# Kernel optimization log

Hardware: AMD Instinct MI355X
Metric: run time of the kernel (lower is better)

## Reference

```python
import jax, jax.numpy as jnp
import numpy as np

T, B, D, H, L = 64, 512, 1536, 1024, 4
DISCOUNT = 0.997
LAM = 0.95


def setup_inputs() -> dict:
    key = jax.random.key(0)
    ks = jax.random.split(key, 3 + L + 1)
    inp = {
        'feat': jax.random.normal(ks[0], (T, B, D), dtype=jnp.float32),
        'reward': jax.random.normal(ks[1], (T - 1, B), dtype=jnp.float32),
        'cont': jnp.ones((T, B), dtype=jnp.float32),
    }
    scale = 0.02
    dims = [D] + [H] * L
    for i in range(L):
        inp[f'W{i}'] = jax.random.normal(ks[3 + i], (dims[i], dims[i + 1]), dtype=jnp.float32) * scale
        inp[f'b{i}'] = jnp.zeros((dims[i + 1],), dtype=jnp.float32)
    inp['Wo'] = jax.random.normal(ks[3 + L], (H,), dtype=jnp.float32) * scale
    inp['bo'] = jnp.zeros((), dtype=jnp.float32)
    return inp


def reference(feat, reward, cont, W0, b0, W1, b1, W2, b2, W3, b3, Wo, bo):
    # Value-net MLP (mean of critic dist): [T, B, D] -> [T, B]
    h = feat
    for W, b in ((W0, b0), (W1, b1), (W2, b2), (W3, b3)):
        h = jax.nn.silu(h @ W + b)
    value = h @ Wo + bo  # [T, B]

    disc = cont[1:] * DISCOUNT                      # [T-1, B]
    deltas = reward + disc * value[1:] - value[:-1]  # [T-1, B]

    # GAE: adv_t = delta_t + disc_t * lambda * adv_{t+1}, adv_T = 0
    def step(adv_next, xs):
        delta, dl = xs
        adv = delta + dl * adv_next
        return adv, adv

    _, advs = jax.lax.scan(step, jnp.zeros_like(value[0]),
                           (deltas, disc * LAM), reverse=True)
    ret = advs + value[:-1]   # lambda-return target, [T-1, B]
    baseline = value[:-1]
    return ret, baseline
```

## Files before the change

### kernel.cpp

```cpp
#include <hip/hip_runtime.h>
#include <hip/hip_bf16.h>

#define T_DIM 64
#define B_DIM 512
#define D_DIM 1536
#define H_DIM 1024
#define M_DIM (T_DIM * B_DIM)
#define DISCOUNT 0.997f
#define LAM 0.95f

#define BM 256
#define BN 256
#define BK 32
#define TILES_M (M_DIM / BM)
#define TILES_N (H_DIM / BN)
#define N_XCD 8

typedef __bf16 bf16x8 __attribute__((ext_vector_type(8)));
typedef float  f32x4  __attribute__((ext_vector_type(4)));

__device__ __forceinline__ void async_load16(const void* g, void* l) {
    __builtin_amdgcn_global_load_lds(
        (const __attribute__((address_space(1))) void*)g,
        (__attribute__((address_space(3))) void*)l,
        16, 0, 0);
}

__device__ __forceinline__ unsigned short f2bf_raw(float f) {
    __hip_bfloat16 h = __float2bfloat16(f);
    return *reinterpret_cast<unsigned short*>(&h);
}

__global__ __launch_bounds__(256) void cvt_bf16_kernel(
    const float* __restrict__ x, __hip_bfloat16* __restrict__ y, long n4) {
    long i = (long)blockIdx.x * blockDim.x + threadIdx.x;
    if (i >= n4) return;
    float4 v = reinterpret_cast<const float4*>(x)[i];
    ushort4 o;
    o.x = f2bf_raw(v.x);
    o.y = f2bf_raw(v.y);
    o.z = f2bf_raw(v.z);
    o.w = f2bf_raw(v.w);
    reinterpret_cast<ushort4*>(y)[i] = o;
}

__global__ __launch_bounds__(256) void transpose_cvt_all_kernel(
    const float* __restrict__ W0, const float* __restrict__ W1,
    const float* __restrict__ W2, const float* __restrict__ W3,
    __hip_bfloat16* __restrict__ T0, __hip_bfloat16* __restrict__ T1,
    __hip_bfloat16* __restrict__ T2, __hip_bfloat16* __restrict__ T3) {
    __shared__ float tile[32][33];
    int z = blockIdx.z;
    const float* W;
    __hip_bfloat16* Tt;
    int K;
    if (z == 0)      { W = W0; Tt = T0; K = D_DIM; }
    else if (z == 1) { W = W1; Tt = T1; K = H_DIM; }
    else if (z == 2) { W = W2; Tt = T2; K = H_DIM; }
    else             { W = W3; Tt = T3; K = H_DIM; }
    int k0 = blockIdx.x * 32, n0 = blockIdx.y * 32;
    if (k0 >= K) return;
    int tx = threadIdx.x, ty = threadIdx.y;
    #pragma unroll
    for (int r = ty; r < 32; r += 8)
        tile[r][tx] = W[(size_t)(k0 + r) * H_DIM + n0 + tx];
    __syncthreads();
    #pragma unroll
    for (int r = ty; r < 32; r += 8)
        Tt[(size_t)(n0 + r) * K + k0 + tx] = __float2bfloat16(tile[tx][r]);
}

__global__ __launch_bounds__(512, 2) void gemm_silu_kernel(
    const __hip_bfloat16* __restrict__ A,
    const __hip_bfloat16* __restrict__ Bt,
    const float* __restrict__ bias,
    __hip_bfloat16* __restrict__ C,
    int K) {

    __shared__ alignas(16) __hip_bfloat16 lds[65536];

    const int tid  = threadIdx.x;
    const int wave = tid >> 6;
    const int lane = tid & 63;
    const int quad = lane >> 4;
    const int r16  = lane & 15;
    const int wm   = wave & 1;
    const int wn   = wave >> 1;

    const int l     = blockIdx.x;
    const int xcd   = l & (N_XCD - 1);
    const int local = l >> 3;
    const int tn    = local & (TILES_N - 1);
    const int tm    = (xcd << 4) | (local >> 2);
    const int m0 = tm * BM;
    const int n0 = tn * BN;

    const int rsub = lane >> 2;
    const int cgrp = lane & 3;
    const int scol = ((cgrp ^ (rsub & 3)) << 3);
    const __hip_bfloat16* gA = A  + (size_t)(m0 + wave * 32 + rsub) * K + scol;
    const __hip_bfloat16* gB = Bt + (size_t)(n0 + wave * 32 + rsub) * K + scol;
    const int ldsOf0 = (wave * 32) * 32;
    const int ldsOf1 = (wave * 32 + 16) * 32;

    const int swz    = ((quad ^ (r16 & 3)) << 3);
    const int rdoffA = (wm * 128 + r16) * 32 + swz;
    const int rdoffB = (wn * 64  + r16) * 32 + swz;

    f32x4 acc[8][4];
    #pragma unroll
    for (int i = 0; i < 8; ++i)
        #pragma unroll
        for (int j = 0; j < 4; ++j)
            acc[i][j] = (f32x4){0.f, 0.f, 0.f, 0.f};

#define STAGE(tt) do { \
        const int sbb = (tt) & 3; \
        __hip_bfloat16* Ab_ = &lds[sbb * 8192]; \
        __hip_bfloat16* Bb_ = &lds[32768 + sbb * 8192]; \
        const size_t ko_ = (size_t)(tt) * BK; \
        async_load16(gA + ko_,                 Ab_ + ldsOf0); \
        async_load16(gA + ko_ + (size_t)16 * K, Ab_ + ldsOf1); \
        async_load16(gB + ko_,                 Bb_ + ldsOf0); \
        async_load16(gB + ko_ + (size_t)16 * K, Bb_ + ldsOf1); \
    } while (0)

#define BODY(t, VMCNT, DOSTAGE) do { \
        asm volatile("s_waitcnt vmcnt(" #VMCNT ")" ::: "memory"); \
        __builtin_amdgcn_s_barrier(); \
        __builtin_amdgcn_sched_barrier(0); \
        const int bb = (t) & 3; \
        const __hip_bfloat16* Ab = &lds[bb * 8192]; \
        const __hip_bfloat16* Bb = &lds[32768 + bb * 8192]; \
        bf16x8 af[8], bfr[4]; \
        _Pragma("unroll") \
        for (int i = 0; i < 8; ++i) \
            af[i] = *reinterpret_cast<const bf16x8*>(Ab + rdoffA + i * 512); \
        _Pragma("unroll") \
        for (int j = 0; j < 4; ++j) \
            bfr[j] = *reinterpret_cast<const bf16x8*>(Bb + rdoffB + j * 512); \
        if (DOSTAGE) STAGE((t) + 3); \
        __builtin_amdgcn_s_setprio(1); \
        _Pragma("unroll") \
        for (int i = 0; i < 8; ++i) \
            _Pragma("unroll") \
            for (int j = 0; j < 4; ++j) \
                acc[i][j] = __builtin_amdgcn_mfma_f32_16x16x32_bf16( \
                    af[i], bfr[j], acc[i][j], 0, 0, 0); \
        __builtin_amdgcn_s_setprio(0); \
    } while (0)

    STAGE(0); STAGE(1); STAGE(2);

    const int NT = K / BK;
    for (int t = 0; t < NT - 2; ++t)
        BODY(t, 8, (t + 3 < NT));
    BODY(NT - 2, 4, false);
    BODY(NT - 1, 0, false);

#undef STAGE
#undef BODY

    #pragma unroll
    for (int j = 0; j < 4; ++j) {
        const int col = n0 + wn * 64 + j * 16 + r16;
        const float bj = bias[col];
        #pragma unroll
        for (int i = 0; i < 8; ++i) {
            const int row_base = m0 + wm * 128 + i * 16 + quad * 4;
            #pragma unroll
            for (int rr = 0; rr < 4; ++rr) {
                const float v = acc[i][j][rr] + bj;
                const float s = v / (1.f + __expf(-v));
                C[(size_t)(row_base + rr) * H_DIM + col] = __float2bfloat16(s);
            }
        }
    }
}

__global__ __launch_bounds__(256) void gemv_value_kernel(
    const __hip_bfloat16* __restrict__ H,
    const float* __restrict__ Wo,
    const float* __restrict__ bo_p,
    float* __restrict__ value, int M) {
    int wave = threadIdx.x >> 6, lane = threadIdx.x & 63;
    int row = blockIdx.x * 4 + wave;
    if (row >= M) return;
    const __hip_bfloat16* hrow = H + (size_t)row * H_DIM;
    float sum = 0.f;
    #pragma unroll
    for (int half = 0; half < 2; ++half) {
        int col = half * 512 + lane * 8;
        uint4 raw = *reinterpret_cast<const uint4*>(hrow + col);
        const __hip_bfloat16* hp = reinterpret_cast<const __hip_bfloat16*>(&raw);
        #pragma unroll
        for (int e = 0; e < 8; ++e)
            sum += __bfloat162float(hp[e]) * Wo[col + e];
    }
    #pragma unroll
    for (int off = 32; off > 0; off >>= 1)
        sum += __shfl_down(sum, off, 64);
    if (lane == 0) value[row] = sum + bo_p[0];
}

__global__ __launch_bounds__(64) void gae_kernel(
    const float* __restrict__ value,
    const float* __restrict__ reward,
    const float* __restrict__ cont,
    float* __restrict__ out) {
    int b = blockIdx.x * blockDim.x + threadIdx.x;
    if (b >= B_DIM) return;
    float adv = 0.f;
    float v_next = value[(T_DIM - 1) * B_DIM + b];
    for (int t = T_DIM - 2; t >= 0; --t) {
        float v_t  = value[t * B_DIM + b];
        float disc = cont[(t + 1) * B_DIM + b] * DISCOUNT;
        float delta = reward[t * B_DIM + b] + disc * v_next - v_t;
        adv = delta + disc * LAM * adv;
        out[t * B_DIM + b] = adv + v_t;
        out[(T_DIM - 1) * B_DIM + t * B_DIM + b] = v_t;
        v_next = v_t;
    }
}

extern "C" void kernel_launch(void* const* d_in, const int* in_sizes, int n_in,
                              void* d_out, int out_size, void* d_ws, size_t ws_size,
                              hipStream_t stream) {
    const float* feat   = (const float*)d_in[0];
    const float* reward = (const float*)d_in[1];
    const float* cont   = (const float*)d_in[2];
    const float* W[4]   = {(const float*)d_in[3], (const float*)d_in[5],
                           (const float*)d_in[7], (const float*)d_in[9]};
    const float* bias[4] = {(const float*)d_in[4], (const float*)d_in[6],
                            (const float*)d_in[8], (const float*)d_in[10]};
    const float* Wo = (const float*)d_in[11];
    const float* bo = (const float*)d_in[12];
    float* out = (float*)d_out;

    char* ws = (char*)d_ws;
    __hip_bfloat16* Xb = (__hip_bfloat16*)ws; ws += (size_t)M_DIM * D_DIM * 2;
    __hip_bfloat16* Ha = (__hip_bfloat16*)ws; ws += (size_t)M_DIM * H_DIM * 2;
    __hip_bfloat16* Hb = (__hip_bfloat16*)ws; ws += (size_t)M_DIM * H_DIM * 2;
    __hip_bfloat16* Wt0 = (__hip_bfloat16*)ws; ws += (size_t)H_DIM * D_DIM * 2;
    __hip_bfloat16* Wt1 = (__hip_bfloat16*)ws; ws += (size_t)H_DIM * H_DIM * 2;
    __hip_bfloat16* Wt2 = (__hip_bfloat16*)ws; ws += (size_t)H_DIM * H_DIM * 2;
    __hip_bfloat16* Wt3 = (__hip_bfloat16*)ws; ws += (size_t)H_DIM * H_DIM * 2;
    float* value = (float*)ws; ws += (size_t)M_DIM * 4;

    long n4 = (long)M_DIM * D_DIM / 4;
    cvt_bf16_kernel<<<(int)((n4 + 255) / 256), 256, 0, stream>>>(feat, Xb, n4);

    transpose_cvt_all_kernel<<<dim3(D_DIM / 32, H_DIM / 32, 4), dim3(32, 8), 0, stream>>>(
        W[0], W[1], W[2], W[3], Wt0, Wt1, Wt2, Wt3);

    const int nblocks = TILES_M * TILES_N;
    gemm_silu_kernel<<<nblocks, 512, 0, stream>>>(Xb, Wt0, bias[0], Ha, D_DIM);
    gemm_silu_kernel<<<nblocks, 512, 0, stream>>>(Ha, Wt1, bias[1], Hb, H_DIM);
    gemm_silu_kernel<<<nblocks, 512, 0, stream>>>(Hb, Wt2, bias[2], Ha, H_DIM);
    gemm_silu_kernel<<<nblocks, 512, 0, stream>>>(Ha, Wt3, bias[3], Hb, H_DIM);

    gemv_value_kernel<<<M_DIM / 4, 256, 0, stream>>>(Hb, Wo, bo, value, M_DIM);

    gae_kernel<<<8, 64, 0, stream>>>(value, reward, cont, out);
}
```

Measured before the change: 717.9 us.

## Interleave LDS fragment reads with MFMAs, swap operands for vectorized epilogue stores

The GEMM inner body now issues the next-stage async global loads right after the barrier. It then splits the A-fragment LDS reads into chunks interleaved with MFMA groups, fenced by sched_barriers and priority hints, which lowers live fragment registers and overlaps LDS latency with math. The LDS swizzle XOR pattern is changed to key on row/2, aimed at reducing bank conflicts. MFMA operands are swapped so each lane holds four consecutive output columns, letting the epilogue do a float4 bias load and a packed 8-byte bf16 store instead of scalar stores. The tighter manual scheduling may constrain the compiler. The swapped layout relies on the helper f2bf_raw existing elsewhere in the file.

```diff
diff --git a/kernel.cpp b/kernel.cpp
--- a/kernel.cpp
+++ b/kernel.cpp
@@ -97,13 +97,13 @@
 
     const int rsub = lane >> 2;
     const int cgrp = lane & 3;
-    const int scol = ((cgrp ^ (rsub & 3)) << 3);
+    const int scol = ((cgrp ^ ((rsub >> 1) & 3)) << 3);
     const __hip_bfloat16* gA = A  + (size_t)(m0 + wave * 32 + rsub) * K + scol;
     const __hip_bfloat16* gB = Bt + (size_t)(n0 + wave * 32 + rsub) * K + scol;
     const int ldsOf0 = (wave * 32) * 32;
     const int ldsOf1 = (wave * 32 + 16) * 32;
 
-    const int swz    = ((quad ^ (r16 & 3)) << 3);
+    const int swz    = ((quad ^ ((r16 >> 1) & 3)) << 3);
     const int rdoffA = (wm * 128 + r16) * 32 + swz;
     const int rdoffB = (wn * 64  + r16) * 32 + swz;
 
@@ -119,35 +119,41 @@
         __hip_bfloat16* Ab_ = &lds[sbb * 8192]; \
         __hip_bfloat16* Bb_ = &lds[32768 + sbb * 8192]; \
         const size_t ko_ = (size_t)(tt) * BK; \
-        async_load16(gA + ko_,                 Ab_ + ldsOf0); \
+        async_load16(gA + ko_,                  Ab_ + ldsOf0); \
         async_load16(gA + ko_ + (size_t)16 * K, Ab_ + ldsOf1); \
-        async_load16(gB + ko_,                 Bb_ + ldsOf0); \
+        async_load16(gB + ko_,                  Bb_ + ldsOf0); \
         async_load16(gB + ko_ + (size_t)16 * K, Bb_ + ldsOf1); \
+    } while (0)
+
+#define RD_A(i) (*reinterpret_cast<const bf16x8*>(Ab + rdoffA + (i) * 512))
+#define RD_B(j) (*reinterpret_cast<const bf16x8*>(Bb + rdoffB + (j) * 512))
+
+#define MM(i, areg) do { \
+        acc[i][0] = __builtin_amdgcn_mfma_f32_16x16x32_bf16(b0, areg, acc[i][0], 0, 0, 0); \
+        acc[i][1] = __builtin_amdgcn_mfma_f32_16x16x32_bf16(b1, areg, acc[i][1], 0, 0, 0); \
+        acc[i][2] = __builtin_amdgcn_mfma_f32_16x16x32_bf16(b2, areg, acc[i][2], 0, 0, 0); \
+        acc[i][3] = __builtin_amdgcn_mfma_f32_16x16x32_bf16(b3, areg, acc[i][3], 0, 0, 0); \
     } while (0)
 
 #define BODY(t, VMCNT, DOSTAGE) do { \
         asm volatile("s_waitcnt vmcnt(" #VMCNT ")" ::: "memory"); \
         __builtin_amdgcn_s_barrier(); \
         __builtin_amdgcn_sched_barrier(0); \
+        if (DOSTAGE) STAGE((t) + 3); \
         const int bb = (t) & 3; \
         const __hip_bfloat16* Ab = &lds[bb * 8192]; \
         const __hip_bfloat16* Bb = &lds[32768 + bb * 8192]; \
-        bf16x8 af[8], bfr[4]; \
-        _Pragma("unroll") \
-        for (int i = 0; i < 8; ++i) \
-            af[i] = *reinterpret_cast<const bf16x8*>(Ab + rdoffA + i * 512); \
-        _Pragma("unroll") \
-        for (int j = 0; j < 4; ++j) \
-            bfr[j] = *reinterpret_cast<const bf16x8*>(Bb + rdoffB + j * 512); \
-        if (DOSTAGE) STAGE((t) + 3); \
-        __builtin_amdgcn_s_setprio(1); \
-        _Pragma("unroll") \
-        for (int i = 0; i < 8; ++i) \
-            _Pragma("unroll") \
-            for (int j = 0; j < 4; ++j) \
-                acc[i][j] = __builtin_amdgcn_mfma_f32_16x16x32_bf16( \
-                    af[i], bfr[j], acc[i][j], 0, 0, 0); \
-        __builtin_amdgcn_s_setprio(0); \
+        bf16x8 b0 = RD_B(0), b1 = RD_B(1), b2 = RD_B(2), b3 = RD_B(3); \
+        bf16x8 a0 = RD_A(0), a1 = RD_A(1), a2 = RD_A(2), a3 = RD_A(3); \
+        __builtin_amdgcn_s_setprio(1); MM(0, a0); MM(1, a1); __builtin_amdgcn_s_setprio(0); \
+        __builtin_amdgcn_sched_barrier(0); \
+        a0 = RD_A(4); a1 = RD_A(5); \
+        __builtin_amdgcn_s_setprio(1); MM(2, a2); MM(3, a3); __builtin_amdgcn_s_setprio(0); \
+        __builtin_amdgcn_sched_barrier(0); \
+        a2 = RD_A(6); a3 = RD_A(7); \
+        __builtin_amdgcn_s_setprio(1); MM(4, a0); MM(5, a1); __builtin_amdgcn_s_setprio(0); \
+        __builtin_amdgcn_sched_barrier(0); \
+        __builtin_amdgcn_s_setprio(1); MM(6, a2); MM(7, a3); __builtin_amdgcn_s_setprio(0); \
     } while (0)
 
     STAGE(0); STAGE(1); STAGE(2);
@@ -159,21 +165,28 @@
     BODY(NT - 1, 0, false);
 
 #undef STAGE
+#undef RD_A
+#undef RD_B
+#undef MM
 #undef BODY
 
     #pragma unroll
     for (int j = 0; j < 4; ++j) {
-        const int col = n0 + wn * 64 + j * 16 + r16;
-        const float bj = bias[col];
+        const int c0 = n0 + wn * 64 + j * 16 + quad * 4;
+        const float4 b4 = *reinterpret_cast<const float4*>(&bias[c0]);
+        const float* bp = reinterpret_cast<const float*>(&b4);
         #pragma unroll
         for (int i = 0; i < 8; ++i) {
-            const int row_base = m0 + wm * 128 + i * 16 + quad * 4;
+            const int row = m0 + wm * 128 + i * 16 + r16;
+            ushort4 o;
+            unsigned short* op = reinterpret_cast<unsigned short*>(&o);
             #pragma unroll
             for (int rr = 0; rr < 4; ++rr) {
-                const float v = acc[i][j][rr] + bj;
+                const float v = acc[i][j][rr] + bp[rr];
                 const float s = v / (1.f + __expf(-v));
-                C[(size_t)(row_base + rr) * H_DIM + col] = __float2bfloat16(s);
+                op[rr] = f2bf_raw(s);
             }
+            *reinterpret_cast<ushort4*>(&C[(size_t)row * H_DIM + c0]) = o;
         }
     }
 }
```

New measurement: 686.8 us. -4.3%, faster.
